# Optimization experiments

Hardware: AMD Instinct MI355X
Metric: run time of the kernel (lower is better)

Reference implementation:

```python
import jax, jax.numpy as jnp
import numpy as np

N_NODES = 30000
N_EDGES = 300000
N_GRAPHS = 512
SEQ = 1000
HEADS = 10
CH = 78


def setup_inputs() -> dict:
    key = jax.random.key(0)
    ks = jax.random.split(key, 20)
    def w(k, shape, scale=0.02):
        return jax.random.normal(k, shape, jnp.float32) * scale
    x = jax.random.normal(ks[0], (N_NODES, CH), jnp.float32)
    edge_index = jax.random.randint(ks[1], (2, N_EDGES), 0, N_NODES, jnp.int32)
    # every graph gets a contiguous block of nodes (sorted batch vector)
    batch = (jnp.arange(N_NODES) * N_GRAPHS // N_NODES).astype(jnp.int32)
    target = jax.random.randint(ks[2], (N_GRAPHS, SEQ), 0, 26, jnp.int32)
    return {
        "x": x, "edge_index": edge_index, "batch": batch, "target": target,
        "W_gat": w(ks[3], (CH, HEADS * CH)),
        "att_src": w(ks[4], (HEADS, CH), 0.1),
        "att_dst": w(ks[5], (HEADS, CH), 0.1),
        "b_gat": jnp.zeros((HEADS * CH,), jnp.float32),
        "W_gcn": w(ks[6], (HEADS * CH, HEADS * CH)),
        "b_gcn": jnp.zeros((HEADS * CH,), jnp.float32),
        "W_fcg1": w(ks[7], (2 * HEADS * CH, 1500)), "b_fcg1": jnp.zeros((1500,), jnp.float32),
        "W_fcg2": w(ks[8], (1500, 128)), "b_fcg2": jnp.zeros((128,), jnp.float32),
        "emb": w(ks[9], (26, 128), 1.0),
        "W_conv": w(ks[10], (32, 1000, 8)), "b_conv": jnp.zeros((32,), jnp.float32),
        "W_fcxt": w(ks[11], (32 * 121, 128)), "b_fcxt": jnp.zeros((128,), jnp.float32),
        "W_fc1": w(ks[12], (256, 1024)), "b_fc1": jnp.zeros((1024,), jnp.float32),
        "W_fc2": w(ks[13], (1024, 512)), "b_fc2": jnp.zeros((512,), jnp.float32),
        "W_out": w(ks[14], (512, 1)), "b_out": jnp.zeros((1,), jnp.float32),
    }


def reference(x, edge_index, batch, target,
              W_gat, att_src, att_dst, b_gat, W_gcn, b_gcn,
              W_fcg1, b_fcg1, W_fcg2, b_fcg2, emb, W_conv, b_conv,
              W_fcxt, b_fcxt, W_fc1, b_fc1, W_fc2, b_fc2, W_out, b_out):
    N = x.shape[0]
    loop = jnp.arange(N, dtype=edge_index.dtype)
    src = jnp.concatenate([edge_index[0], loop])  # self-loops (PyG default)
    dst = jnp.concatenate([edge_index[1], loop])

    # ---- GATConv(78 -> 78, heads=10, concat) ----
    h = (x @ W_gat).reshape(N, HEADS, CH)           # [N,H,C]
    a_s = jnp.einsum('nhc,hc->nh', h, att_src)      # [N,H]
    a_d = jnp.einsum('nhc,hc->nh', h, att_dst)
    logits = jax.nn.leaky_relu(a_s[src] + a_d[dst], 0.2)   # [E',H]
    m = jax.ops.segment_max(logits, dst, num_segments=N)
    e = jnp.exp(logits - m[dst])
    denom = jax.ops.segment_sum(e, dst, num_segments=N)
    alpha = e / (denom[dst] + 1e-16)                # per-dst softmax
    xg = jax.ops.segment_sum(h[src] * alpha[:, :, None], dst, num_segments=N)
    xg = jax.nn.relu(xg.reshape(N, HEADS * CH) + b_gat)

    # ---- GCNConv(780 -> 780), symmetric norm with self-loops ----
    deg = jax.ops.segment_sum(jnp.ones_like(dst, dtype=xg.dtype), dst, num_segments=N)
    dinv = jax.lax.rsqrt(jnp.maximum(deg, 1.0))
    norm = dinv[src] * dinv[dst]                    # [E']
    xw = xg @ W_gcn
    xg = jax.ops.segment_sum(xw[src] * norm[:, None], dst, num_segments=N) + b_gcn
    xg = jax.nn.relu(xg)

    # ---- global max + mean pooling per graph ----
    gmax = jax.ops.segment_max(xg, batch, num_segments=N_GRAPHS)
    cnt = jax.ops.segment_sum(jnp.ones((N,), xg.dtype), batch, num_segments=N_GRAPHS)
    gmean = jax.ops.segment_sum(xg, batch, num_segments=N_GRAPHS) / cnt[:, None]
    xp = jnp.concatenate([gmax, gmean], axis=1)     # [G,1560]
    xp = jax.nn.relu(xp @ W_fcg1 + b_fcg1)          # dropout = identity (eval)
    xp = xp @ W_fcg2 + b_fcg2                       # [G,128]

    # ---- protein branch ----
    xt = emb[target]                                # [G,1000,128]
    conv = jax.lax.conv_general_dilated(
        xt, W_conv, window_strides=(1,), padding='VALID',
        dimension_numbers=('NCH', 'OIH', 'NCH'))    # [G,32,121]
    conv = conv + b_conv[None, :, None]
    xt = conv.reshape(conv.shape[0], -1) @ W_fcxt + b_fcxt  # [G,128]

    # ---- joint MLP ----
    xc = jnp.concatenate([xp, xt], axis=1)          # [G,256]
    xc = jax.nn.relu(xc @ W_fc1 + b_fc1)
    xc = jax.nn.relu(xc @ W_fc2 + b_fc2)
    return xc @ W_out + b_out                       # [G,1]
```

## Files before the change

kernel.cpp:

```cpp
#include <hip/hip_runtime.h>
#include <hip/hip_bf16.h>
#include <cstdint>
#include <cstddef>

#define N_NODES 30000
#define E0      300000
#define EPRIME  330000
#define NG      512
#define SEQL    1000
#define HEADS   10
#define CHN     78
#define HC      780
#define HP      800
#define MAXD    64

typedef __attribute__((ext_vector_type(8))) short bf16x8;
typedef __attribute__((ext_vector_type(4))) float f32x4;

static __device__ __forceinline__ int src_of(const int* ei, int e){
  return (e < E0) ? ei[e] : (e - E0);
}
static __device__ __forceinline__ int dst_of(const int* ei, int e){
  return (e < E0) ? ei[E0 + e] : (e - E0);
}
static __device__ __forceinline__ unsigned short f2bf(float f){
  union { float f; unsigned u; } a; a.f = f;
  unsigned r = a.u + 0x7fff + ((a.u >> 16) & 1);
  return (unsigned short)(r >> 16);
}
static __device__ __forceinline__ float bf2f(unsigned short u){
  union { unsigned u; float f; } a; a.u = ((unsigned)u) << 16; return a.f;
}
static __device__ __forceinline__ void gl_lds16(const unsigned short* g, unsigned short* l){
  __builtin_amdgcn_global_load_lds(
      (const __attribute__((address_space(1))) void*)g,
      (__attribute__((address_space(3))) void*)l,
      16, 0, 0);
}

__global__ void k_bucket(const int* __restrict__ ei, int* __restrict__ cnt, int* __restrict__ bkt){
  int e = blockIdx.x*256 + threadIdx.x;
  if (e < EPRIME){
    int d = dst_of(ei, e);
    int s = src_of(ei, e);
    int slot = atomicAdd(&cnt[d], 1);
    if (slot < MAXD) bkt[d*MAXD + slot] = s;
  }
}

static __device__ void transp_tile(const float* __restrict__ src, unsigned short* __restrict__ dst,
                                   int K, int N, int Kp, int bx, int by){
  __shared__ float t[32][33];
  int k0 = bx*32, n0 = by*32;
  int c = threadIdx.x & 31, r = threadIdx.x >> 5;
  #pragma unroll
  for (int i=0;i<4;i++){
    int k = k0 + r + i*8;
    float v = 0.f;
    if (k < K && n0 + c < N) v = src[(size_t)k*N + n0 + c];
    t[r + i*8][c] = v;
  }
  __syncthreads();
  #pragma unroll
  for (int i=0;i<4;i++){
    int nn = n0 + r + i*8;
    int kk = k0 + c;
    if (nn < N && kk < Kp) dst[(size_t)nn*Kp + kk] = f2bf(t[c][r + i*8]);
  }
}

__global__ __launch_bounds__(256) void k_prep(
    const float* __restrict__ x, unsigned short* __restrict__ xb,
    const float* __restrict__ W_gat, unsigned short* __restrict__ wgat_t,
    const float* __restrict__ W_gcn, unsigned short* __restrict__ wgcn_t,
    const float* __restrict__ W_fcg1, unsigned short* __restrict__ wfcg1_t,
    float* __restrict__ xc, float* __restrict__ t1, float* __restrict__ t2, float* __restrict__ fg1,
    const float* __restrict__ b_fcg2, const float* __restrict__ b_fcxt,
    const float* __restrict__ b_fc1, const float* __restrict__ b_fc2,
    const float* __restrict__ b_fcg1, int* __restrict__ cnt)
{
  int b = blockIdx.x;
  int tid = threadIdx.x;
  if (b < 11250){
    int idx = b*256 + tid;
    if (idx < N_NODES*96){
      int n = idx/96, k = idx - n*96;
      xb[idx] = (k < CHN) ? f2bf(x[(size_t)n*CHN + k]) : 0;
    }
    return;
  }
  b -= 11250;
  if (b < 75){ transp_tile(W_gat, wgat_t, CHN, HC, 96, b%3, b/3); return; }
  b -= 75;
  if (b < 625){ transp_tile(W_gcn, wgcn_t, HC, HC, HP, b%25, b/25); return; }
  b -= 625;
  if (b < 2303){ transp_tile(W_fcg1, wfcg1_t, 1560, 1500, 1568, b%49, b/49); return; }
  b -= 2303;
  int g = b;
  int zi = g*256 + tid;
  if (zi < N_NODES) cnt[zi] = 0;
  if (tid < 128){
    xc[(size_t)g*256 + tid]       = b_fcg2[tid];
    xc[(size_t)g*256 + 128 + tid] = b_fcxt[tid];
  }
  for (int i = tid; i < 1024; i += 256) t1[(size_t)g*1024 + i] = b_fc1[i];
  for (int i = tid; i < 512;  i += 256) t2[(size_t)g*512  + i] = b_fc2[i];
  for (int i = tid; i < 1500; i += 256) fg1[(size_t)g*1500 + i] = b_fcg1[i];
}

__global__ __launch_bounds__(256) void k_mfma_bt(
    const unsigned short* __restrict__ A, const unsigned short* __restrict__ Bt,
    const float* __restrict__ bias, float* __restrict__ C, unsigned short* __restrict__ Cb,
    int M, int N, int Kp, int ldc, int relu,
    int ntc, int ntr, int ntk, int Kc, int accum)
{
  const int total = ntc*ntr*ntk;
  const int per = (total + 7) >> 3;
  const int b = blockIdx.x;
  const int w = (b & 7)*per + (b >> 3);
  if (w >= total) return;
  const int kt = w / (ntc*ntr);
  const int r2 = w - kt*(ntc*ntr);
  const int row_t = r2 / ntc, col_t = r2 - row_t*ntc;
  const int row0 = row_t*128, col0 = col_t*128;
  const int kbeg = kt*Kc;
  const int kend = min(kbeg + Kc, Kp);

  __shared__ unsigned short As[128*32];
  __shared__ unsigned short Bs[128*32];
  const int tid = threadIdx.x;
  const int lane = tid & 63;
  const int wv = tid >> 6;
  const int wm = wv >> 1, wn = wv & 1;
  const int quad = lane >> 4, l16 = lane & 15;
  const int srow = lane >> 2;
  const int scol = (lane & 3) * 8;

  f32x4 acc[4][4];
  #pragma unroll
  for (int mi=0;mi<4;mi++)
    #pragma unroll
    for (int ni=0;ni<4;ni++){
      acc[mi][ni][0]=0.f; acc[mi][ni][1]=0.f; acc[mi][ni][2]=0.f; acc[mi][ni][3]=0.f;
    }

  for (int k0 = kbeg; k0 < kend; k0 += 32){
    #pragma unroll
    for (int i=0;i<2;i++){
      int ch = wv*2 + i;
      int r  = ch*16 + srow;
      gl_lds16(A  + (size_t)(row0 + r)*Kp + k0 + scol, &As[ch*512]);
      gl_lds16(Bt + (size_t)(col0 + r)*Kp + k0 + scol, &Bs[ch*512]);
    }
    __syncthreads();
    bf16x8 af[4], bfr[4];
    #pragma unroll
    for (int mi=0;mi<4;mi++) af[mi]  = *(const bf16x8*)(&As[(wm*64 + mi*16 + l16)*32 + quad*8]);
    #pragma unroll
    for (int ni=0;ni<4;ni++) bfr[ni] = *(const bf16x8*)(&Bs[(wn*64 + ni*16 + l16)*32 + quad*8]);
    #pragma unroll
    for (int mi=0;mi<4;mi++)
      #pragma unroll
      for (int ni=0;ni<4;ni++)
        acc[mi][ni] = __builtin_amdgcn_mfma_f32_16x16x32_bf16(af[mi], bfr[ni], acc[mi][ni], 0,0,0);
    __syncthreads();
  }

  #pragma unroll
  for (int mi=0;mi<4;mi++){
    #pragma unroll
    for (int rr=0;rr<4;rr++){
      int row = row0 + wm*64 + mi*16 + quad*4 + rr;
      if (row >= M) continue;
      #pragma unroll
      for (int ni=0;ni<4;ni++){
        int col = col0 + wn*64 + ni*16 + l16;
        if (col >= N) continue;
        float v = acc[mi][ni][rr];
        if (accum){
          atomicAdd(&C[(size_t)row*ldc + col], v);
        } else {
          if (bias) v += bias[col];
          if (relu) v = fmaxf(v, 0.f);
          if (Cb) Cb[(size_t)row*ldc + col] = f2bf(v);
          else    C [(size_t)row*ldc + col] = v;
        }
      }
    }
  }
}

__global__ __launch_bounds__(256) void k_gemm_sk(const float* __restrict__ A, const float* __restrict__ B,
    float* __restrict__ C, int M, int N, int K, int lda, int ldb, int ldc, int Kc, int relu_a)
{
  __shared__ float As[16][34];
  __shared__ float Bs[16][64];
  const int tid = threadIdx.x;
  const int tx = tid & 15, ty = tid >> 4;
  const int row0 = blockIdx.y * 32, col0 = blockIdx.x * 64;
  const int kbeg = blockIdx.z * Kc;
  const int kend = min(kbeg + Kc, K);
  float acc[2][4];
  #pragma unroll
  for (int i=0;i<2;i++)
    #pragma unroll
    for (int j=0;j<4;j++) acc[i][j] = 0.f;

  for (int k0 = kbeg; k0 < kend; k0 += 16){
    #pragma unroll
    for (int i=0;i<2;i++){
      int idx = tid + i*256;
      int r = idx >> 4, c = idx & 15;
      int gr = row0 + r, gc = k0 + c;
      float v = (gr < M && gc < kend) ? A[(size_t)gr*lda + gc] : 0.f;
      if (relu_a) v = fmaxf(v, 0.f);
      As[c][r] = v;
    }
    #pragma unroll
    for (int i=0;i<4;i++){
      int idx = tid + i*256;
      int r = idx >> 6, c = idx & 63;
      int gr = k0 + r, gc = col0 + c;
      Bs[r][c] = (gr < kend && gc < N) ? B[(size_t)gr*ldb + gc] : 0.f;
    }
    __syncthreads();
    #pragma unroll
    for (int kk=0; kk<16; kk++){
      float a0 = As[kk][ty*2], a1 = As[kk][ty*2+1];
      float b0 = Bs[kk][tx*4], b1 = Bs[kk][tx*4+1], b2 = Bs[kk][tx*4+2], b3 = Bs[kk][tx*4+3];
      acc[0][0]+=a0*b0; acc[0][1]+=a0*b1; acc[0][2]+=a0*b2; acc[0][3]+=a0*b3;
      acc[1][0]+=a1*b0; acc[1][1]+=a1*b1; acc[1][2]+=a1*b2; acc[1][3]+=a1*b3;
    }
    __syncthreads();
  }
  #pragma unroll
  for (int i=0;i<2;i++){
    int r = row0 + ty*2 + i;
    if (r >= M) continue;
    #pragma unroll
    for (int j=0;j<4;j++){
      int c = col0 + tx*4 + j;
      if (c < N) atomicAdd(&C[(size_t)r*ldc + c], acc[i][j]);
    }
  }
}

__global__ __launch_bounds__(256) void k_attn(const unsigned short* __restrict__ hb,
    const float* __restrict__ att_src, const float* __restrict__ att_dst,
    float* __restrict__ a_s, float* __restrict__ a_d){
  __shared__ float ssrc[HC], sdst[HC];
  for (int i = threadIdx.x; i < HC; i += 256){ ssrc[i]=att_src[i]; sdst[i]=att_dst[i]; }
  __syncthreads();
  int idx = blockIdx.x*256 + threadIdx.x;
  if (idx >= N_NODES*HEADS) return;
  int hh = idx % HEADS;
  const unsigned* hp2 = (const unsigned*)(hb + (size_t)idx*CHN);
  const float* as_ = ssrc + hh*CHN;
  const float* ad_ = sdst + hh*CHN;
  float s1=0.f, s2=0.f;
  #pragma unroll 13
  for (int c2=0;c2<39;c2++){
    unsigned u = hp2[c2];
    float v0 = bf2f((unsigned short)(u & 0xffffu));
    float v1 = bf2f((unsigned short)(u >> 16));
    int c = 2*c2;
    s1 += v0*as_[c] + v1*as_[c+1];
    s2 += v0*ad_[c] + v1*ad_[c+1];
  }
  a_s[idx]=s1; a_d[idx]=s2;
}

__global__ __launch_bounds__(256) void k_gat_agg(
    const unsigned short* __restrict__ hb, const float* __restrict__ a_s, const float* __restrict__ a_d,
    const float* __restrict__ b_gat, const int* __restrict__ cnt, const int* __restrict__ bkt,
    unsigned short* __restrict__ xgb, float* __restrict__ dinv)
{
  int n = blockIdx.x;
  int deg = cnt[n];
  int degc = min(deg, MAXD);
  int tid = threadIdx.x;
  __shared__ int   s_src[MAXD];
  __shared__ float s_adn[HEADS];
  __shared__ float s_lg[MAXD*HEADS];
  __shared__ float s_al[MAXD*HEADS];
  if (tid < HEADS) s_adn[tid] = a_d[(size_t)n*HEADS + tid];
  if (tid < degc)  s_src[tid] = bkt[n*MAXD + tid];
  __syncthreads();
  for (int idx = tid; idx < degc*HEADS; idx += 256){
    int j = idx/HEADS, t = idx - j*HEADS;
    float l = a_s[(size_t)s_src[j]*HEADS + t] + s_adn[t];
    s_lg[idx] = (l > 0.f) ? l : 0.2f*l;
  }
  __syncthreads();
  if (tid < HEADS){
    float m = -3.4e38f;
    for (int j=0;j<degc;j++) m = fmaxf(m, s_lg[j*HEADS+tid]);
    float s = 0.f;
    for (int j=0;j<degc;j++){ float e = __expf(s_lg[j*HEADS+tid]-m); s_al[j*HEADS+tid]=e; s+=e; }
    float inv = 1.f/(s + 1e-16f);
    for (int j=0;j<degc;j++) s_al[j*HEADS+tid] *= inv;
  }
  __syncthreads();
  int c = tid;
  if (c < 195){
    int ch = 4*c;
    int h0 = ch/CHN, h1 = (ch+1)/CHN, h2 = (ch+2)/CHN, h3 = (ch+3)/CHN;
    float ax=0.f, ay=0.f, az=0.f, aw=0.f;
    const ushort4* h4 = (const ushort4*)hb;
    for (int j=0;j<degc;j++){
      ushort4 v = h4[(size_t)s_src[j]*195 + c];
      const float* al = &s_al[j*HEADS];
      ax += al[h0]*bf2f(v.x); ay += al[h1]*bf2f(v.y);
      az += al[h2]*bf2f(v.z); aw += al[h3]*bf2f(v.w);
    }
    ushort4 o;
    o.x = f2bf(fmaxf(ax + b_gat[ch+0], 0.f));
    o.y = f2bf(fmaxf(ay + b_gat[ch+1], 0.f));
    o.z = f2bf(fmaxf(az + b_gat[ch+2], 0.f));
    o.w = f2bf(fmaxf(aw + b_gat[ch+3], 0.f));
    *(ushort4*)(xgb + (size_t)n*HP + ch) = o;
  } else if (c < 200){
    ushort4 z = {0,0,0,0};
    *(ushort4*)(xgb + (size_t)n*HP + 4*c) = z;
  }
  if (tid == 0) dinv[n] = rsqrtf((float)deg);
}

__global__ __launch_bounds__(256) void k_gcn_agg(
    const unsigned short* __restrict__ xwb, const float* __restrict__ dinv, const float* __restrict__ b_gcn,
    const int* __restrict__ cnt, const int* __restrict__ bkt,
    unsigned short* __restrict__ xg2b)
{
  int n = blockIdx.x;
  int deg = min(cnt[n], MAXD);
  int tid = threadIdx.x;
  __shared__ int   s_src[MAXD];
  __shared__ float s_w[MAXD];
  if (tid < deg){
    int s = bkt[n*MAXD + tid];
    s_src[tid] = s;
    s_w[tid] = dinv[s];
  }
  __syncthreads();
  if (tid < 195){
    float ax=0.f, ay=0.f, az=0.f, aw=0.f;
    const ushort4* x4 = (const ushort4*)xwb;
    for (int j=0;j<deg;j++){
      ushort4 v = x4[(size_t)s_src[j]*195 + tid];
      float w = s_w[j];
      ax += w*bf2f(v.x); ay += w*bf2f(v.y); az += w*bf2f(v.z); aw += w*bf2f(v.w);
    }
    float dn = dinv[n];
    int ch = 4*tid;
    ushort4 o;
    o.x = f2bf(fmaxf(dn*ax + b_gcn[ch+0], 0.f));
    o.y = f2bf(fmaxf(dn*ay + b_gcn[ch+1], 0.f));
    o.z = f2bf(fmaxf(dn*az + b_gcn[ch+2], 0.f));
    o.w = f2bf(fmaxf(dn*aw + b_gcn[ch+3], 0.f));
    *(ushort4*)(xg2b + (size_t)n*HC + ch) = o;
  }
}

__global__ __launch_bounds__(256) void k_pool(const unsigned short* __restrict__ xg2b,
                                              unsigned short* __restrict__ xpb){
  int g = blockIdx.x;
  int n0 = (N_NODES*g + NG-1) >> 9;
  int n1 = (N_NODES*(g+1) + NG-1) >> 9;
  float inv = 1.f/(float)(n1 - n0);
  int c4 = threadIdx.x;
  if (c4 < 195){
    const ushort4* x4 = (const ushort4*)xg2b;
    float m0=-3.4e38f,m1=-3.4e38f,m2=-3.4e38f,m3=-3.4e38f;
    float s0=0.f,s1=0.f,s2=0.f,s3=0.f;
    for (int n = n0; n < n1; n++){
      ushort4 v = x4[(size_t)n*195 + c4];
      float a=bf2f(v.x), b=bf2f(v.y), c=bf2f(v.z), d=bf2f(v.w);
      m0=fmaxf(m0,a); m1=fmaxf(m1,b); m2=fmaxf(m2,c); m3=fmaxf(m3,d);
      s0+=a; s1+=b; s2+=c; s3+=d;
    }
    int ch = 4*c4;
    unsigned short* row = xpb + (size_t)g*1568;
    row[ch]=f2bf(m0); row[ch+1]=f2bf(m1); row[ch+2]=f2bf(m2); row[ch+3]=f2bf(m3);
    row[HC+ch]=f2bf(s0*inv); row[HC+ch+1]=f2bf(s1*inv);
    row[HC+ch+2]=f2bf(s2*inv); row[HC+ch+3]=f2bf(s3*inv);
  }
  if (threadIdx.x < 8) xpb[(size_t)g*1568 + 1560 + threadIdx.x] = 0;
}

__global__ __launch_bounds__(256) void k_conv(const int* __restrict__ target, const float* __restrict__ W_conv,
                                              const float* __restrict__ emb, const float* __restrict__ b_conv,
                                              float* __restrict__ convf){
  int g = blockIdx.x;
  int tid = threadIdx.x;
  int o = tid >> 3, k = tid & 7;
  __shared__ float U[256*26];
  __shared__ float sE[26*128 + 32];
  #pragma unroll
  for (int j=0;j<26;j++) U[tid*26+j] = 0.f;
  for (int i = tid; i < 26*128; i += 256) sE[i] = emb[i];
  if (tid < 32) sE[26*128 + tid] = 0.f;
  const int* tg = target + g*SEQL;
  const float* wp = W_conv + o*8000 + k;
  for (int i=0;i<SEQL;i++){
    int v = tg[i];
    U[tid*26 + v] += wp[i*8];
  }
  __syncthreads();
  int pg = tid & 7;
  int p0 = pg * 16;
  int np = 121 - p0; if (np > 16) np = 16;
  float acc[16];
  #pragma unroll
  for (int i=0;i<16;i++) acc[i]=0.f;
  for (int v = 0; v < 26; v++){
    float u[8];
    #pragma unroll
    for (int kk=0;kk<8;kk++) u[kk] = U[(o*8 + kk)*26 + v];
    const float* ep = &sE[v*128 + p0];
    float e[24];
    #pragma unroll
    for (int i=0;i<24;i+=4){
      float4 q = *(const float4*)(ep + i);
      e[i]=q.x; e[i+1]=q.y; e[i+2]=q.z; e[i+3]=q.w;
    }
    #pragma unroll
    for (int pl=0; pl<16; pl++){
      acc[pl] += u[0]*e[pl]   + u[1]*e[pl+1] + u[2]*e[pl+2] + u[3]*e[pl+3]
               + u[4]*e[pl+4] + u[5]*e[pl+5] + u[6]*e[pl+6] + u[7]*e[pl+7];
    }
  }
  float bo = b_conv[o];
  for (int pl=0; pl<np; pl++)
    convf[(size_t)g*3872 + o*121 + p0 + pl] = acc[pl] + bo;
}

__global__ __launch_bounds__(64) void k_final(const float* __restrict__ t2, const float* __restrict__ W_out,
                                              const float* __restrict__ b_out, float* __restrict__ out){
  int g = blockIdx.x;
  int lane = threadIdx.x;
  const float* r = t2 + (size_t)g*512;
  float s = 0.f;
  #pragma unroll
  for (int i = lane; i < 512; i += 64) s += fmaxf(r[i], 0.f)*W_out[i];
  #pragma unroll
  for (int off=32; off; off>>=1) s += __shfl_down(s, off);
  if (lane==0) out[g] = s + b_out[0];
}

extern "C" void kernel_launch(void* const* d_in, const int* in_sizes, int n_in,
                              void* d_out, int out_size, void* d_ws, size_t ws_size,
                              hipStream_t stream) {
  const float* x      = (const float*)d_in[0];
  const int*   ei     = (const int*)  d_in[1];
  const int*   target = (const int*)  d_in[3];
  const float* W_gat  = (const float*)d_in[4];
  const float* att_src= (const float*)d_in[5];
  const float* att_dst= (const float*)d_in[6];
  const float* b_gat  = (const float*)d_in[7];
  const float* W_gcn  = (const float*)d_in[8];
  const float* b_gcn  = (const float*)d_in[9];
  const float* W_fcg1 = (const float*)d_in[10];
  const float* b_fcg1 = (const float*)d_in[11];
  const float* W_fcg2 = (const float*)d_in[12];
  const float* b_fcg2 = (const float*)d_in[13];
  const float* emb    = (const float*)d_in[14];
  const float* W_conv = (const float*)d_in[15];
  const float* b_conv = (const float*)d_in[16];
  const float* W_fcxt = (const float*)d_in[17];
  const float* b_fcxt = (const float*)d_in[18];
  const float* W_fc1  = (const float*)d_in[19];
  const float* b_fc1  = (const float*)d_in[20];
  const float* W_fc2  = (const float*)d_in[21];
  const float* b_fc2  = (const float*)d_in[22];
  const float* W_out  = (const float*)d_in[23];
  const float* b_out  = (const float*)d_in[24];
  float* out = (float*)d_out;

  char* ws = (char*)d_ws;
  size_t off = 0;
  auto alloc = [&](size_t bytes)->char*{
    char* p = ws + off;
    off += (bytes + 255) & ~(size_t)255;
    return p;
  };
  unsigned short* hb  = (unsigned short*)alloc((size_t)N_NODES*HC*2);
  unsigned short* xwb = (unsigned short*)alloc((size_t)N_NODES*HC*2);
  unsigned short* xu  = (unsigned short*)alloc((size_t)N_NODES*HP*2);
  unsigned short* xb     = (unsigned short*)alloc((size_t)N_NODES*96*2);
  unsigned short* wgat_t = (unsigned short*)alloc((size_t)HC*96*2);
  unsigned short* wgcn_t = (unsigned short*)alloc((size_t)HC*HP*2);
  unsigned short* wfcg1_t= (unsigned short*)alloc((size_t)1500*1568*2);
  unsigned short* xpb    = (unsigned short*)alloc((size_t)NG*1568*2);
  float* a_s    = (float*)alloc((size_t)N_NODES*HEADS*4);
  float* a_d    = (float*)alloc((size_t)N_NODES*HEADS*4);
  float* dinv   = (float*)alloc((size_t)N_NODES*4);
  int*   cnt    = (int*)  alloc((size_t)N_NODES*4);
  int*   bkt    = (int*)  alloc((size_t)N_NODES*MAXD*4);
  float* fg1    = (float*)alloc((size_t)NG*1500*4);
  float* convf  = (float*)alloc((size_t)NG*3872*4);
  float* xc     = (float*)alloc((size_t)NG*256*4);
  float* t1     = (float*)alloc((size_t)NG*1024*4);
  float* t2     = (float*)alloc((size_t)NG*512*4);

  unsigned short* xgb  = xu;
  unsigned short* xg2b = xu;

  k_prep<<<11250+75+625+2303+512, 256, 0, stream>>>(
      x, xb, W_gat, wgat_t, W_gcn, wgcn_t, W_fcg1, wfcg1_t,
      xc, t1, t2, fg1, b_fcg2, b_fcxt, b_fc1, b_fc2, b_fcg1, cnt);

  k_bucket<<<(EPRIME+255)/256, 256, 0, stream>>>(ei, cnt, bkt);

  auto swgrid = [](int total){ return 8 * ((total + 7) / 8); };

  k_mfma_bt<<<swgrid(7*235), 256, 0, stream>>>(xb, wgat_t, nullptr, nullptr, hb,
                                               N_NODES, HC, 96, HC, 0, 7, 235, 1, 96, 0);
  k_attn<<<(N_NODES*HEADS+255)/256, 256, 0, stream>>>(hb, att_src, att_dst, a_s, a_d);
  k_gat_agg<<<N_NODES, 256, 0, stream>>>(hb, a_s, a_d, b_gat, cnt, bkt, xgb, dinv);

  k_mfma_bt<<<swgrid(7*235), 256, 0, stream>>>(xgb, wgcn_t, nullptr, nullptr, xwb,
                                               N_NODES, HC, HP, HC, 0, 7, 235, 1, HP, 0);
  k_gcn_agg<<<N_NODES, 256, 0, stream>>>(xwb, dinv, b_gcn, cnt, bkt, xg2b);

  k_pool<<<NG, 256, 0, stream>>>(xg2b, xpb);
  k_mfma_bt<<<swgrid(12*4*2), 256, 0, stream>>>(xpb, wfcg1_t, nullptr, fg1, nullptr,
                                                NG, 1500, 1568, 1500, 0, 12, 4, 2, 800, 1);
  k_gemm_sk<<<dim3(2, 16, 8), 256, 0, stream>>>(fg1, W_fcg2, xc, NG, 128, 1500, 1500, 128, 256, 192, 1);

  k_conv<<<NG, 256, 0, stream>>>(target, W_conv, emb, b_conv, convf);
  k_gemm_sk<<<dim3(2, 16, 8), 256, 0, stream>>>(convf, W_fcxt, xc + 128, NG, 128, 3872, 3872, 128, 256, 512, 0);

  k_gemm_sk<<<dim3(16, 16, 1), 256, 0, stream>>>(xc, W_fc1, t1, NG, 1024, 256, 256, 1024, 1024, 256, 0);
  k_gemm_sk<<<dim3(8, 16, 2), 256, 0, stream>>>(t1, W_fc2, t2, NG, 512, 1024, 1024, 512, 512, 512, 1);
  k_final<<<NG, 64, 0, stream>>>(t2, W_out, b_out, out);
}
```

Measured before the change: 838.6 us.

## Counting-sort protein tokens and transpose conv weights for coalesced histogram build

Adds a prep stage that transposes W_conv into a [position][o*8+k] layout so consecutive threads read contiguous weights. The conv kernel now stages the target sequence in shared memory, counting-sorts the positions by token value, and has each thread accumulate per-token sums in registers before writing U once. This replaces 1000 scattered read-modify-write shared-memory updates per thread and strided global weight loads. In exchange it adds shared-memory atomics, extra barriers and a serial prefix step on one thread.

```diff
diff --git a/kernel.cpp b/kernel.cpp
--- a/kernel.cpp
+++ b/kernel.cpp
@@ -16,6 +16,7 @@
 
 typedef __attribute__((ext_vector_type(8))) short bf16x8;
 typedef __attribute__((ext_vector_type(4))) float f32x4;
+typedef __attribute__((ext_vector_type(8))) unsigned short u16x8;
 
 static __device__ __forceinline__ int src_of(const int* ei, int e){
   return (e < E0) ? ei[e] : (e - E0);
@@ -74,6 +75,7 @@
     const float* __restrict__ W_gat, unsigned short* __restrict__ wgat_t,
     const float* __restrict__ W_gcn, unsigned short* __restrict__ wgcn_t,
     const float* __restrict__ W_fcg1, unsigned short* __restrict__ wfcg1_t,
+    const float* __restrict__ W_conv, float* __restrict__ w2t,
     float* __restrict__ xc, float* __restrict__ t1, float* __restrict__ t2, float* __restrict__ fg1,
     const float* __restrict__ b_fcg2, const float* __restrict__ b_fcxt,
     const float* __restrict__ b_fc1, const float* __restrict__ b_fc2,
@@ -96,16 +98,24 @@
   b -= 625;
   if (b < 2303){ transp_tile(W_fcg1, wfcg1_t, 1560, 1500, 1568, b%49, b/49); return; }
   b -= 2303;
-  int g = b;
-  int zi = g*256 + tid;
-  if (zi < N_NODES) cnt[zi] = 0;
-  if (tid < 128){
-    xc[(size_t)g*256 + tid]       = b_fcg2[tid];
-    xc[(size_t)g*256 + 128 + tid] = b_fcxt[tid];
-  }
-  for (int i = tid; i < 1024; i += 256) t1[(size_t)g*1024 + i] = b_fc1[i];
-  for (int i = tid; i < 512;  i += 256) t2[(size_t)g*512  + i] = b_fc2[i];
-  for (int i = tid; i < 1500; i += 256) fg1[(size_t)g*1500 + i] = b_fcg1[i];
+  if (b < 512){
+    int g = b;
+    int zi = g*256 + tid;
+    if (zi < N_NODES) cnt[zi] = 0;
+    if (tid < 128){
+      xc[(size_t)g*256 + tid]       = b_fcg2[tid];
+      xc[(size_t)g*256 + 128 + tid] = b_fcxt[tid];
+    }
+    for (int i = tid; i < 1024; i += 256) t1[(size_t)g*1024 + i] = b_fc1[i];
+    for (int i = tid; i < 512;  i += 256) t2[(size_t)g*512  + i] = b_fc2[i];
+    for (int i = tid; i < 1500; i += 256) fg1[(size_t)g*1500 + i] = b_fcg1[i];
+    return;
+  }
+  b -= 512;
+  {
+    int o = tid >> 3, k = tid & 7;
+    w2t[(size_t)b*256 + tid] = W_conv[(size_t)o*8000 + b*8 + k];
+  }
 }
 
 __global__ __launch_bounds__(256) void k_mfma_bt(
@@ -387,25 +397,69 @@
   if (threadIdx.x < 8) xpb[(size_t)g*1568 + 1560 + threadIdx.x] = 0;
 }
 
-__global__ __launch_bounds__(256) void k_conv(const int* __restrict__ target, const float* __restrict__ W_conv,
+__global__ __launch_bounds__(256) void k_conv(const int* __restrict__ target,
+                                              const float* __restrict__ W2t,
                                               const float* __restrict__ emb, const float* __restrict__ b_conv,
                                               float* __restrict__ convf){
   int g = blockIdx.x;
   int tid = threadIdx.x;
-  int o = tid >> 3, k = tid & 7;
+  int o = tid >> 3;
+  __shared__ int   tgt[SEQL];
+  __shared__ int   cntv[26];
+  __shared__ int   startv[27];
+  __shared__ int   ofs[26];
+  __shared__ alignas(16) unsigned short posv[SEQL];
   __shared__ float U[256*26];
   __shared__ float sE[26*128 + 32];
-  #pragma unroll
-  for (int j=0;j<26;j++) U[tid*26+j] = 0.f;
+
   for (int i = tid; i < 26*128; i += 256) sE[i] = emb[i];
   if (tid < 32) sE[26*128 + tid] = 0.f;
+  if (tid < 26) cntv[tid] = 0;
   const int* tg = target + g*SEQL;
-  const float* wp = W_conv + o*8000 + k;
-  for (int i=0;i<SEQL;i++){
-    int v = tg[i];
-    U[tid*26 + v] += wp[i*8];
-  }
-  __syncthreads();
+  for (int i = tid; i < SEQL; i += 256) tgt[i] = tg[i];
+  __syncthreads();
+
+  for (int i = tid; i < SEQL; i += 256) atomicAdd(&cntv[tgt[i]], 1);
+  __syncthreads();
+  if (tid == 0){
+    int s = 0;
+    #pragma unroll
+    for (int v = 0; v < 26; v++){ startv[v] = s; ofs[v] = s; s += cntv[v]; }
+    startv[26] = s;
+  }
+  __syncthreads();
+  for (int i = tid; i < SEQL; i += 256){
+    int v = tgt[i];
+    int slot = atomicAdd(&ofs[v], 1);
+    posv[slot] = (unsigned short)((v << 10) | i);
+  }
+  __syncthreads();
+
+  {
+    const float* wp2 = W2t + tid;
+    float s = 0.f;
+    int cur = 0;
+    for (int j = 0; j < SEQL; j += 8){
+      u16x8 p8 = *(const u16x8*)&posv[j];
+      float w[8];
+      #pragma unroll
+      for (int q = 0; q < 8; q++) w[q] = wp2[((int)p8[q] & 1023) << 8];
+      #pragma unroll
+      for (int q = 0; q < 8; q++){
+        int ve = (int)p8[q] >> 10;
+        if (ve != cur){
+          U[tid*26 + cur] = s;
+          for (int z = cur+1; z < ve; z++) U[tid*26 + z] = 0.f;
+          cur = ve; s = 0.f;
+        }
+        s += w[q];
+      }
+    }
+    U[tid*26 + cur] = s;
+    for (int z = cur+1; z < 26; z++) U[tid*26 + z] = 0.f;
+  }
+  __syncthreads();
+
   int pg = tid & 7;
   int p0 = pg * 16;
   int np = 121 - p0; if (np > 16) np = 16;
@@ -501,12 +555,13 @@
   float* xc     = (float*)alloc((size_t)NG*256*4);
   float* t1     = (float*)alloc((size_t)NG*1024*4);
   float* t2     = (float*)alloc((size_t)NG*512*4);
+  float* w2t    = (float*)alloc((size_t)SEQL*256*4);
 
   unsigned short* xgb  = xu;
   unsigned short* xg2b = xu;
 
-  k_prep<<<11250+75+625+2303+512, 256, 0, stream>>>(
-      x, xb, W_gat, wgat_t, W_gcn, wgcn_t, W_fcg1, wfcg1_t,
+  k_prep<<<11250+75+625+2303+512+1000, 256, 0, stream>>>(
+      x, xb, W_gat, wgat_t, W_gcn, wgcn_t, W_fcg1, wfcg1_t, W_conv, w2t,
       xc, t1, t2, fg1, b_fcg2, b_fcxt, b_fc1, b_fc2, b_fcg1, cnt);
 
   k_bucket<<<(EPRIME+255)/256, 256, 0, stream>>>(ei, cnt, bkt);
@@ -527,7 +582,7 @@
                                                 NG, 1500, 1568, 1500, 0, 12, 4, 2, 800, 1);
   k_gemm_sk<<<dim3(2, 16, 8), 256, 0, stream>>>(fg1, W_fcg2, xc, NG, 128, 1500, 1500, 128, 256, 192, 1);
 
-  k_conv<<<NG, 256, 0, stream>>>(target, W_conv, emb, b_conv, convf);
+  k_conv<<<NG, 256, 0, stream>>>(target, w2t, emb, b_conv, convf);
   k_gemm_sk<<<dim3(2, 16, 8), 256, 0, stream>>>(convf, W_fcxt, xc + 128, NG, 128, 3872, 3872, 128, 256, 512, 0);
 
   k_gemm_sk<<<dim3(16, 16, 1), 256, 0, stream>>>(xc, W_fc1, t1, NG, 1024, 256, 256, 1024, 1024, 256, 0);
```

Measured after the change: 826.3 us. No clear change (-1.5%).
